# Kernel tuning notes

Hardware: AMD Instinct MI355X
Metric: run time of the kernel (lower is better)

The kernel has to match this reference:

```python
import jax, jax.numpy as jnp
import numpy as np

H, I, B, S = 3200, 12800, 8, 1024  # InternViT-6B MLP dims


def setup_inputs() -> dict:
    key = jax.random.key(0)
    ks = jax.random.split(key, 8)
    # int8-valued activations/weights stored as int32 (harness dtype set)
    hidden_states = jax.random.randint(ks[0], (B, S, H), -127, 128, dtype=jnp.int32)
    scale = jax.random.uniform(ks[1], (B * S,), dtype=jnp.float32) * 1e-3 + 1e-5
    w1 = jax.random.randint(ks[2], (I, H), -127, 128, dtype=jnp.int32)
    w1_scale = jax.random.uniform(ks[3], (I,), dtype=jnp.float32) * 1e-3 + 1e-5
    b1 = jax.random.normal(ks[4], (I,), dtype=jnp.float32) * 0.02
    w2 = jax.random.randint(ks[5], (H, I), -127, 128, dtype=jnp.int32)
    w2_scale = jax.random.uniform(ks[6], (H,), dtype=jnp.float32) * 1e-3 + 1e-5
    b2 = jax.random.normal(ks[7], (H,), dtype=jnp.float32) * 0.02
    return {"hidden_states": hidden_states, "scale": scale, "w1": w1,
            "w1_scale": w1_scale, "b1": b1, "w2": w2, "w2_scale": w2_scale, "b2": b2}


def _w8a8_linear(x_q, x_scale, w_q, w_scale, b):
    # enough that fp32 matmul reproduces the exact integer accumulator to
    # within float32 rounding of the final sum.
    acc = jnp.matmul(x_q.astype(jnp.float32), w_q.astype(jnp.float32).T)  # [T, out]
    out = acc * x_scale[:, None] * w_scale[None, :] + b[None, :]
    return out.astype(jnp.float16)


def reference(hidden_states, scale, w1, w1_scale, b1, w2, w2_scale, b2):
    bsz, seq, hidden = hidden_states.shape
    x_q = hidden_states.reshape(-1, hidden)                 # [T, H] int8 values
    # fc1: W8A8 -> fp16 with dynamic per-token input scale
    fc1_out = _w8a8_linear(x_q, scale, w1, w1_scale, b1)    # [T, I] fp16
    # fused gelu_and_quant: exact GELU, then per-token dynamic int8 re-quant
    g = jax.nn.gelu(fc1_out.astype(jnp.float32), approximate=False)  # [T, I]
    new_scale = jnp.max(jnp.abs(g), axis=-1) / 127.0        # dynamic per-token scale
    act_q = jnp.clip(jnp.round(g / new_scale[:, None]), -127, 127)  # int8 values
    # fc2: W8A8 -> fp16
    out = _w8a8_linear(act_q, new_scale, w2, w2_scale, b2)  # [T, H] fp16
    return out
```

## Files before the change

kernel.cpp:

```cpp
#include <hip/hip_runtime.h>
#include <hip/hip_bf16.h>
#include <hip/hip_fp16.h>

#define T_DIM 8192
#define H_DIM 3200
#define I_DIM 12800

typedef int v4i __attribute__((ext_vector_type(4)));
typedef _Float16 h8 __attribute__((ext_vector_type(8)));

__device__ __forceinline__ void gload16(const void* g, void* l) {
    __builtin_amdgcn_global_load_lds(
        (const __attribute__((address_space(1))) unsigned int*)g,
        (__attribute__((address_space(3))) unsigned int*)l, 16, 0, 0);
}

__global__ __launch_bounds__(256) void repack_kernel(const int* __restrict__ src,
                                                     unsigned int* __restrict__ dst,
                                                     long n4) {
    long i = (long)blockIdx.x * blockDim.x + threadIdx.x;
    long stride = (long)gridDim.x * blockDim.x;
    for (; i < n4; i += stride) {
        int4 v = ((const int4*)src)[i];
        dst[i] = (unsigned int)((v.x & 255) | ((v.y & 255) << 8) |
                                ((v.z & 255) << 16) | ((v.w & 255) << 24));
    }
}

template <int EPI>
__global__ __launch_bounds__(1024, 4) void gemm_i8_16w(
    const signed char* __restrict__ A, long strideA,
    const signed char* __restrict__ B, long strideB,
    int Ntrue, int K, int ldc,
    const float* __restrict__ rowscale, const float* __restrict__ colscale,
    const float* __restrict__ bias, void* __restrict__ Cout) {
    __shared__ signed char lds[131072];
    signed char* ldsA = lds;
    signed char* ldsB = lds + 65536;

    const int tid = threadIdx.x;
    const int lane = tid & 63, wid = tid >> 6;
    const int wr = wid >> 2, wc = wid & 3;
    const int bm = blockIdx.x, bn = blockIdx.y;
    const long Arow0 = (long)bm * 256;
    const long Bcol0 = (long)bn * 256;

    const int r0 = tid >> 2;
    const int s0 = (((tid & 3) ^ ((r0 >> 1) & 3)) << 4);
    const signed char* Ag0 = A + (Arow0 + r0) * strideA + s0;
    const signed char* Bg0 = B + (Bcol0 + r0) * strideB + s0;
    const int d0 = tid * 16;

    const int NH = K >> 6;

#define STAGE_AB(h)                                 \
    {                                               \
        const int hc_ = (h) < NH ? (h) : NH - 1;    \
        const long ko_ = (long)hc_ << 6;            \
        const int sl_ = ((h) & 3) << 14;            \
        gload16(Ag0 + ko_, ldsA + sl_ + d0);        \
        gload16(Bg0 + ko_, ldsB + sl_ + d0);        \
    }

    const int r = lane & 15, q = lane >> 4;
    const int swz = ((q ^ ((r >> 1) & 3)) << 4);
    const int aoff = (wr * 64 + r) * 64 + swz;
    const int boff = (wc * 64 + r) * 64 + swz;

    v4i acc[4][4] = {};
    v4i af[4], bf[4];

    STAGE_AB(0); STAGE_AB(1); STAGE_AB(2);
    asm volatile("s_waitcnt vmcnt(4)");
    __builtin_amdgcn_s_barrier();

    for (int h = 0; h < NH; ++h) {
        const signed char* sA = ldsA + ((h & 3) << 14);
        const signed char* sB = ldsB + ((h & 3) << 14);
#pragma unroll
        for (int i = 0; i < 4; ++i) af[i] = *(const v4i*)(sA + aoff + i * 1024);
#pragma unroll
        for (int n = 0; n < 4; ++n) bf[n] = *(const v4i*)(sB + boff + n * 1024);
        STAGE_AB(h + 3);
        __builtin_amdgcn_s_setprio(1);
#pragma unroll
        for (int m = 0; m < 4; ++m)
#pragma unroll
            for (int n = 0; n < 4; ++n)
                acc[m][n] = __builtin_amdgcn_mfma_i32_16x16x64_i8(
                    af[m], bf[n], acc[m][n], 0, 0, 0);
        __builtin_amdgcn_s_setprio(0);
        asm volatile("s_waitcnt vmcnt(4)");
        __builtin_amdgcn_s_barrier();
    }

    const int row0 = bm * 256 + wr * 64;
    const int col0 = bn * 256 + wc * 64;
    const int r4 = (lane >> 4) << 2, cl = lane & 15;
#pragma unroll
    for (int m = 0; m < 4; ++m) {
        const int rowb = row0 + m * 16 + r4;
        float rs[4];
#pragma unroll
        for (int rr = 0; rr < 4; ++rr) rs[rr] = rowscale[rowb + rr];
#pragma unroll
        for (int n = 0; n < 4; ++n) {
            const int col = col0 + n * 16 + cl;
            if (col < Ntrue) {
                const float cs = colscale[col];
                const float bs = bias[col];
#pragma unroll
                for (int rr = 0; rr < 4; ++rr) {
                    float v = (float)acc[m][n][rr];
                    v = __fmul_rn(v, rs[rr]);
                    v = __fmul_rn(v, cs);
                    v = __fadd_rn(v, bs);
                    _Float16 hh = (_Float16)v;
                    const size_t idx = (size_t)(rowb + rr) * ldc + col;
                    if (EPI == 0) ((_Float16*)Cout)[idx] = hh;
                    else ((float*)Cout)[idx] = (float)hh;
                }
            }
        }
    }
#undef STAGE_AB
}

__global__ __launch_bounds__(256) void gelu_quant(_Float16* __restrict__ fc1,
                                                  float* __restrict__ nscale) {
    __shared__ float gbuf[I_DIM];
    __shared__ float wmax[4];
    const int tid = threadIdx.x, lane = tid & 63, wid = tid >> 6;
    const long t = blockIdx.x;
    const h8* row = (const h8*)(fc1 + t * I_DIM);
    float lmax = 0.f;
    for (int c = tid; c < I_DIM / 8; c += 256) {
        h8 v = row[c];
#pragma unroll
        for (int j = 0; j < 8; ++j) {
            float x = (float)v[j];
            float e = erff(__fdiv_rn(x, 1.41421356237309504880f));
            float g = __fmul_rn(__fmul_rn(0.5f, x), __fadd_rn(1.0f, e));
            gbuf[c * 8 + j] = g;
            lmax = fmaxf(lmax, fabsf(g));
        }
    }
#pragma unroll
    for (int off = 32; off; off >>= 1) lmax = fmaxf(lmax, __shfl_xor(lmax, off, 64));
    if (lane == 0) wmax[wid] = lmax;
    __syncthreads();
    const float gmax = fmaxf(fmaxf(wmax[0], wmax[1]), fmaxf(wmax[2], wmax[3]));
    const float ns = gmax / 127.0f;
    if (tid == 0) nscale[t] = ns;
    unsigned long long* out = (unsigned long long*)(fc1 + t * I_DIM);
    for (int c = tid; c < I_DIM / 8; c += 256) {
        unsigned long long pk = 0;
#pragma unroll
        for (int j = 0; j < 8; ++j) {
            float qv = rintf(__fdiv_rn(gbuf[c * 8 + j], ns));
            qv = fminf(fmaxf(qv, -127.f), 127.f);
            pk |= ((unsigned long long)(unsigned char)(signed char)(int)qv) << (8 * j);
        }
        out[c] = pk;
    }
}

extern "C" void kernel_launch(void* const* d_in, const int* in_sizes, int n_in,
                              void* d_out, int out_size, void* d_ws, size_t ws_size,
                              hipStream_t stream) {
    const int* hs = (const int*)d_in[0];
    const float* scale = (const float*)d_in[1];
    const int* w1 = (const int*)d_in[2];
    const float* w1s = (const float*)d_in[3];
    const float* b1 = (const float*)d_in[4];
    const int* w2 = (const int*)d_in[5];
    const float* w2s = (const float*)d_in[6];
    const float* b2 = (const float*)d_in[7];

    char* ws = (char*)d_ws;
    signed char* xq = (signed char*)ws;
    signed char* w1q = xq + (size_t)T_DIM * H_DIM;
    signed char* w2q = w1q + (size_t)I_DIM * H_DIM;
    _Float16* fc1h = (_Float16*)(w2q + (size_t)H_DIM * I_DIM);
    const size_t fixed = (size_t)T_DIM * H_DIM + 2 * (size_t)I_DIM * H_DIM;

    int nc = 1;
    while (nc < 16) {
        size_t need = fixed + ((size_t)T_DIM / nc) * I_DIM * 2 +
                      ((size_t)T_DIM / nc) * 4 + 256;
        if (need <= ws_size) break;
        nc <<= 1;
    }
    const int chunkT = T_DIM / nc;
    float* nscale = (float*)((char*)fc1h + (size_t)chunkT * I_DIM * 2);

    repack_kernel<<<2048, 256, 0, stream>>>(hs, (unsigned int*)xq, (long)T_DIM * H_DIM / 4);
    repack_kernel<<<2048, 256, 0, stream>>>(w1, (unsigned int*)w1q, (long)I_DIM * H_DIM / 4);
    repack_kernel<<<2048, 256, 0, stream>>>(w2, (unsigned int*)w2q, (long)H_DIM * I_DIM / 4);

    const int n2tiles = (H_DIM + 255) / 256;
    for (int c = 0; c < nc; ++c) {
        const int t0 = c * chunkT;
        gemm_i8_16w<0><<<dim3(chunkT / 256, I_DIM / 256), 1024, 0, stream>>>(
            xq + (size_t)t0 * H_DIM, (long)H_DIM, w1q, (long)H_DIM,
            I_DIM, H_DIM, I_DIM,
            scale + t0, w1s, b1, (void*)fc1h);
        gelu_quant<<<chunkT, 256, 0, stream>>>(fc1h, nscale);
        gemm_i8_16w<1><<<dim3(chunkT / 256, n2tiles), 1024, 0, stream>>>(
            (const signed char*)fc1h, (long)I_DIM * 2, w2q, (long)I_DIM,
            H_DIM, I_DIM, H_DIM,
            nscale, w2s, b2,
            (void*)((float*)d_out + (size_t)t0 * H_DIM));
    }
}
```

Before: 949.1 us.

## Restructure int8 GEMM K-loop into double-buffered 128-wide pair stages

The GEMM main loop used to stage 64-wide K slices into a 4-slot LDS ring, three slices ahead, with a barrier after every slice. It now stages two 64-wide halves at once into one of two 32 KB buffers and computes both halves before a single barrier. This halves the number of barriers and waitcnt points per K. The cost is shallower prefetch: only one pair is in flight, and each phase waits with vmcnt(0), so global-load latency is less well hidden.

```diff
diff --git a/kernel.cpp b/kernel.cpp
--- a/kernel.cpp
+++ b/kernel.cpp
@@ -28,7 +28,7 @@
 }
 
 template <int EPI>
-__global__ __launch_bounds__(1024, 4) void gemm_i8_16w(
+__global__ __launch_bounds__(1024, 4) void gemm_i8_pair(
     const signed char* __restrict__ A, long strideA,
     const signed char* __restrict__ B, long strideB,
     int Ntrue, int K, int ldc,
@@ -51,15 +51,15 @@
     const signed char* Bg0 = B + (Bcol0 + r0) * strideB + s0;
     const int d0 = tid * 16;
 
-    const int NH = K >> 6;
-
-#define STAGE_AB(h)                                 \
-    {                                               \
-        const int hc_ = (h) < NH ? (h) : NH - 1;    \
-        const long ko_ = (long)hc_ << 6;            \
-        const int sl_ = ((h) & 3) << 14;            \
-        gload16(Ag0 + ko_, ldsA + sl_ + d0);        \
-        gload16(Bg0 + ko_, ldsB + sl_ + d0);        \
+    const int NP = K >> 7;
+
+#define STAGE_PAIR(p, SB)                             \
+    {                                                 \
+        const long ko_ = (long)(p) << 7;              \
+        gload16(Ag0 + ko_, ldsA + (SB) + d0);         \
+        gload16(Bg0 + ko_, ldsB + (SB) + d0);         \
+        gload16(Ag0 + ko_ + 64, ldsA + (SB) + 16384 + d0); \
+        gload16(Bg0 + ko_ + 64, ldsB + (SB) + 16384 + d0); \
     }
 
     const int r = lane & 15, q = lane >> 4;
@@ -68,30 +68,38 @@
     const int boff = (wc * 64 + r) * 64 + swz;
 
     v4i acc[4][4] = {};
-    v4i af[4], bf[4];
-
-    STAGE_AB(0); STAGE_AB(1); STAGE_AB(2);
-    asm volatile("s_waitcnt vmcnt(4)");
+
+#define HALF(HB)                                                            \
+    {                                                                       \
+        v4i af[4], bf[4];                                                   \
+        _Pragma("unroll") for (int i = 0; i < 4; ++i)                       \
+            af[i] = *(const v4i*)(ldsA + (HB) + aoff + i * 1024);           \
+        _Pragma("unroll") for (int n = 0; n < 4; ++n)                       \
+            bf[n] = *(const v4i*)(ldsB + (HB) + boff + n * 1024);           \
+        __builtin_amdgcn_s_setprio(1);                                      \
+        _Pragma("unroll") for (int m = 0; m < 4; ++m)                       \
+            _Pragma("unroll") for (int n = 0; n < 4; ++n)                   \
+                acc[m][n] = __builtin_amdgcn_mfma_i32_16x16x64_i8(          \
+                    af[m], bf[n], acc[m][n], 0, 0, 0);                      \
+        __builtin_amdgcn_s_setprio(0);                                      \
+    }
+
+#define PAIR_PHASE(SB, OTHER, DO_STAGE, pn)        \
+    {                                              \
+        if (DO_STAGE) STAGE_PAIR(pn, OTHER);       \
+        HALF(SB);                                  \
+        HALF((SB) + 16384);                        \
+        asm volatile("s_waitcnt vmcnt(0)");        \
+        __builtin_amdgcn_s_barrier();              \
+    }
+
+    STAGE_PAIR(0, 0);
+    asm volatile("s_waitcnt vmcnt(0)");
     __builtin_amdgcn_s_barrier();
 
-    for (int h = 0; h < NH; ++h) {
-        const signed char* sA = ldsA + ((h & 3) << 14);
-        const signed char* sB = ldsB + ((h & 3) << 14);
-#pragma unroll
-        for (int i = 0; i < 4; ++i) af[i] = *(const v4i*)(sA + aoff + i * 1024);
-#pragma unroll
-        for (int n = 0; n < 4; ++n) bf[n] = *(const v4i*)(sB + boff + n * 1024);
-        STAGE_AB(h + 3);
-        __builtin_amdgcn_s_setprio(1);
-#pragma unroll
-        for (int m = 0; m < 4; ++m)
-#pragma unroll
-            for (int n = 0; n < 4; ++n)
-                acc[m][n] = __builtin_amdgcn_mfma_i32_16x16x64_i8(
-                    af[m], bf[n], acc[m][n], 0, 0, 0);
-        __builtin_amdgcn_s_setprio(0);
-        asm volatile("s_waitcnt vmcnt(4)");
-        __builtin_amdgcn_s_barrier();
+    for (int p = 0; p < NP; p += 2) {
+        PAIR_PHASE(0, 32768, p + 1 < NP, p + 1);
+        if (p + 1 < NP) PAIR_PHASE(32768, 0, p + 2 < NP, p + 2);
     }
 
     const int row0 = bm * 256 + wr * 64;
@@ -123,7 +131,9 @@
             }
         }
     }
-#undef STAGE_AB
+#undef PAIR_PHASE
+#undef HALF
+#undef STAGE_PAIR
 }
 
 __global__ __launch_bounds__(256) void gelu_quant(_Float16* __restrict__ fc1,
@@ -201,12 +211,12 @@
     const int n2tiles = (H_DIM + 255) / 256;
     for (int c = 0; c < nc; ++c) {
         const int t0 = c * chunkT;
-        gemm_i8_16w<0><<<dim3(chunkT / 256, I_DIM / 256), 1024, 0, stream>>>(
+        gemm_i8_pair<0><<<dim3(chunkT / 256, I_DIM / 256), 1024, 0, stream>>>(
             xq + (size_t)t0 * H_DIM, (long)H_DIM, w1q, (long)H_DIM,
             I_DIM, H_DIM, I_DIM,
             scale + t0, w1s, b1, (void*)fc1h);
         gelu_quant<<<chunkT, 256, 0, stream>>>(fc1h, nscale);
-        gemm_i8_16w<1><<<dim3(chunkT / 256, n2tiles), 1024, 0, stream>>>(
+        gemm_i8_pair<1><<<dim3(chunkT / 256, n2tiles), 1024, 0, stream>>>(
             (const signed char*)fc1h, (long)I_DIM * 2, w2q, (long)I_DIM,
             H_DIM, I_DIM, H_DIM,
             nscale, w2s, b2,
```

New measurement: 951.9 us. No clear change (+0.3%).

## Shrink GEMM tile to 128x256 with triple-buffered LDS and register-resident GELU

Applied to the files above, without the earlier changes.

The int8 GEMM moves from 1024-thread 256x256 tiles with four LDS stages (128KB) to 512-thread 128x256 tiles with three rotating LDS stages (72KB). This should let two blocks share a CU and doubles the grid size along the token dimension. The prefetch distance drops from 3 to 2 stages and the vmcnt waits change to match, so there is less latency hiding per block and B tiles are reloaded more often. Separately, gelu_quant uses 320 threads and keeps each row's GELU values in registers rather than a 50KB shared buffer, which raises occupancy for that kernel.

```diff
diff --git a/kernel.cpp b/kernel.cpp
--- a/kernel.cpp
+++ b/kernel.cpp
@@ -28,38 +28,41 @@
 }
 
 template <int EPI>
-__global__ __launch_bounds__(1024, 4) void gemm_i8_16w(
+__global__ __launch_bounds__(512, 4) void gemm_i8_2cu(
     const signed char* __restrict__ A, long strideA,
     const signed char* __restrict__ B, long strideB,
     int Ntrue, int K, int ldc,
     const float* __restrict__ rowscale, const float* __restrict__ colscale,
     const float* __restrict__ bias, void* __restrict__ Cout) {
-    __shared__ signed char lds[131072];
+    __shared__ signed char lds[73728];
     signed char* ldsA = lds;
-    signed char* ldsB = lds + 65536;
+    signed char* ldsB = lds + 24576;
 
     const int tid = threadIdx.x;
     const int lane = tid & 63, wid = tid >> 6;
     const int wr = wid >> 2, wc = wid & 3;
     const int bm = blockIdx.x, bn = blockIdx.y;
-    const long Arow0 = (long)bm * 256;
+    const long Arow0 = (long)bm * 128;
     const long Bcol0 = (long)bn * 256;
 
-    const int r0 = tid >> 2;
-    const int s0 = (((tid & 3) ^ ((r0 >> 1) & 3)) << 4);
-    const signed char* Ag0 = A + (Arow0 + r0) * strideA + s0;
-    const signed char* Bg0 = B + (Bcol0 + r0) * strideB + s0;
-    const int d0 = tid * 16;
+    const int rA = tid >> 2;
+    const int sA = (((tid & 3) ^ ((rA >> 1) & 3)) << 4);
+    const int rB1 = 128 + (tid >> 2);
+    const int sB1 = (((tid & 3) ^ ((rB1 >> 1) & 3)) << 4);
+    const signed char* Ag0 = A + (Arow0 + rA) * strideA + sA;
+    const signed char* Bg0 = B + (Bcol0 + rA) * strideB + sA;
+    const signed char* Bg1 = B + (Bcol0 + rB1) * strideB + sB1;
+    const int dA = tid * 16, dB0 = tid * 16, dB1 = (tid + 512) * 16;
 
     const int NH = K >> 6;
 
-#define STAGE_AB(h)                                 \
+#define STAGE(h, soA_, soB_)                        \
     {                                               \
         const int hc_ = (h) < NH ? (h) : NH - 1;    \
         const long ko_ = (long)hc_ << 6;            \
-        const int sl_ = ((h) & 3) << 14;            \
-        gload16(Ag0 + ko_, ldsA + sl_ + d0);        \
-        gload16(Bg0 + ko_, ldsB + sl_ + d0);        \
+        gload16(Ag0 + ko_, ldsA + (soA_) + dA);     \
+        gload16(Bg0 + ko_, ldsB + (soB_) + dB0);    \
+        gload16(Bg1 + ko_, ldsB + (soB_) + dB1);    \
     }
 
     const int r = lane & 15, q = lane >> 4;
@@ -70,18 +73,21 @@
     v4i acc[4][4] = {};
     v4i af[4], bf[4];
 
-    STAGE_AB(0); STAGE_AB(1); STAGE_AB(2);
-    asm volatile("s_waitcnt vmcnt(4)");
+    STAGE(0, 0, 0);
+    STAGE(1, 8192, 16384);
+    asm volatile("s_waitcnt vmcnt(3)");
     __builtin_amdgcn_s_barrier();
 
+    int soAc = 0, soAn = 8192, soAs = 16384;
+    int soBc = 0, soBn = 16384, soBs = 32768;
     for (int h = 0; h < NH; ++h) {
-        const signed char* sA = ldsA + ((h & 3) << 14);
-        const signed char* sB = ldsB + ((h & 3) << 14);
-#pragma unroll
-        for (int i = 0; i < 4; ++i) af[i] = *(const v4i*)(sA + aoff + i * 1024);
-#pragma unroll
-        for (int n = 0; n < 4; ++n) bf[n] = *(const v4i*)(sB + boff + n * 1024);
-        STAGE_AB(h + 3);
+        const signed char* sAp = ldsA + soAc;
+        const signed char* sBp = ldsB + soBc;
+#pragma unroll
+        for (int i = 0; i < 4; ++i) af[i] = *(const v4i*)(sAp + aoff + i * 1024);
+#pragma unroll
+        for (int n = 0; n < 4; ++n) bf[n] = *(const v4i*)(sBp + boff + n * 1024);
+        STAGE(h + 2, soAs, soBs);
         __builtin_amdgcn_s_setprio(1);
 #pragma unroll
         for (int m = 0; m < 4; ++m)
@@ -90,11 +96,13 @@
                 acc[m][n] = __builtin_amdgcn_mfma_i32_16x16x64_i8(
                     af[m], bf[n], acc[m][n], 0, 0, 0);
         __builtin_amdgcn_s_setprio(0);
-        asm volatile("s_waitcnt vmcnt(4)");
+        asm volatile("s_waitcnt vmcnt(3)");
         __builtin_amdgcn_s_barrier();
-    }
-
-    const int row0 = bm * 256 + wr * 64;
+        const int tA = soAc; soAc = soAn; soAn = soAs; soAs = tA;
+        const int tB = soBc; soBc = soBn; soBn = soBs; soBs = tB;
+    }
+
+    const int row0 = bm * 128 + wr * 64;
     const int col0 = bn * 256 + wc * 64;
     const int r4 = (lane >> 4) << 2, cl = lane & 15;
 #pragma unroll
@@ -123,45 +131,48 @@
             }
         }
     }
-#undef STAGE_AB
-}
-
-__global__ __launch_bounds__(256) void gelu_quant(_Float16* __restrict__ fc1,
+#undef STAGE
+}
+
+__global__ __launch_bounds__(320) void gelu_quant(_Float16* __restrict__ fc1,
                                                   float* __restrict__ nscale) {
-    __shared__ float gbuf[I_DIM];
-    __shared__ float wmax[4];
+    __shared__ float wmax[5];
     const int tid = threadIdx.x, lane = tid & 63, wid = tid >> 6;
     const long t = blockIdx.x;
     const h8* row = (const h8*)(fc1 + t * I_DIM);
+    float g[5][8];
     float lmax = 0.f;
-    for (int c = tid; c < I_DIM / 8; c += 256) {
-        h8 v = row[c];
+#pragma unroll
+    for (int k = 0; k < 5; ++k) {
+        h8 v = row[tid + k * 320];
 #pragma unroll
         for (int j = 0; j < 8; ++j) {
             float x = (float)v[j];
             float e = erff(__fdiv_rn(x, 1.41421356237309504880f));
-            float g = __fmul_rn(__fmul_rn(0.5f, x), __fadd_rn(1.0f, e));
-            gbuf[c * 8 + j] = g;
-            lmax = fmaxf(lmax, fabsf(g));
+            float gg = __fmul_rn(__fmul_rn(0.5f, x), __fadd_rn(1.0f, e));
+            g[k][j] = gg;
+            lmax = fmaxf(lmax, fabsf(gg));
         }
     }
 #pragma unroll
     for (int off = 32; off; off >>= 1) lmax = fmaxf(lmax, __shfl_xor(lmax, off, 64));
     if (lane == 0) wmax[wid] = lmax;
     __syncthreads();
-    const float gmax = fmaxf(fmaxf(wmax[0], wmax[1]), fmaxf(wmax[2], wmax[3]));
+    const float gmax = fmaxf(fmaxf(fmaxf(wmax[0], wmax[1]), fmaxf(wmax[2], wmax[3])),
+                             wmax[4]);
     const float ns = gmax / 127.0f;
     if (tid == 0) nscale[t] = ns;
     unsigned long long* out = (unsigned long long*)(fc1 + t * I_DIM);
-    for (int c = tid; c < I_DIM / 8; c += 256) {
+#pragma unroll
+    for (int k = 0; k < 5; ++k) {
         unsigned long long pk = 0;
 #pragma unroll
         for (int j = 0; j < 8; ++j) {
-            float qv = rintf(__fdiv_rn(gbuf[c * 8 + j], ns));
+            float qv = rintf(__fdiv_rn(g[k][j], ns));
             qv = fminf(fmaxf(qv, -127.f), 127.f);
             pk |= ((unsigned long long)(unsigned char)(signed char)(int)qv) << (8 * j);
         }
-        out[c] = pk;
+        out[tid + k * 320] = pk;
     }
 }
 
@@ -201,12 +212,12 @@
     const int n2tiles = (H_DIM + 255) / 256;
     for (int c = 0; c < nc; ++c) {
         const int t0 = c * chunkT;
-        gemm_i8_16w<0><<<dim3(chunkT / 256, I_DIM / 256), 1024, 0, stream>>>(
+        gemm_i8_2cu<0><<<dim3(chunkT / 128, I_DIM / 256), 512, 0, stream>>>(
             xq + (size_t)t0 * H_DIM, (long)H_DIM, w1q, (long)H_DIM,
             I_DIM, H_DIM, I_DIM,
             scale + t0, w1s, b1, (void*)fc1h);
-        gelu_quant<<<chunkT, 256, 0, stream>>>(fc1h, nscale);
-        gemm_i8_16w<1><<<dim3(chunkT / 256, n2tiles), 1024, 0, stream>>>(
+        gelu_quant<<<chunkT, 320, 0, stream>>>(fc1h, nscale);
+        gemm_i8_2cu<1><<<dim3(chunkT / 128, n2tiles), 512, 0, stream>>>(
             (const signed char*)fc1h, (long)I_DIM * 2, w2q, (long)I_DIM,
             H_DIM, I_DIM, H_DIM,
             nscale, w2s, b2,
```

Result: slower. 1.103 ms (+16.2%).
